# Performance work log

Measured on AMD Instinct MI355X. Metric: run time of the kernel, lower is better.

## Reference

```python
import jax, jax.numpy as jnp
import numpy as np
from jax import lax

B, C, H, W = 2, 96, 64, 64
D_INNER, D_STATE, DT_RANK, K = 192, 16, 6, 4
EPS = 1e-5


def _ln(x, g, b):
    mu = jnp.mean(x, -1, keepdims=True)
    var = jnp.var(x, -1, keepdims=True)
    return (x - mu) * lax.rsqrt(var + EPS) * g + b


def setup_inputs() -> dict:
    key = jax.random.key(0)
    ks = jax.random.split(key, 10)
    f = lambda k, s, sc=0.02: jax.random.normal(k, s, dtype=jnp.float32) * sc
    return {
        "rgb": jax.random.normal(ks[0], (B, C, H, W), dtype=jnp.float32),
        "t": jax.random.normal(ks[1], (B, C, H, W), dtype=jnp.float32),
        "conv_w": f(ks[2], (C, 2 * C, 3, 3), 0.05),
        "conv_b": jnp.zeros((C,), jnp.float32),
        "bn_gamma": jnp.ones((C,), jnp.float32),
        "bn_beta": jnp.zeros((C,), jnp.float32),
        "bn_mean": jnp.zeros((C,), jnp.float32),
        "bn_var": jnp.ones((C,), jnp.float32),
        "ln_gamma": jnp.ones((C,), jnp.float32),
        "ln_beta": jnp.zeros((C,), jnp.float32),
        "in_proj_w": f(ks[3], (2 * D_INNER, C)),
        "dwconv_w": f(ks[4], (D_INNER, 1, 3, 3), 0.1),
        "dwconv_b": jnp.zeros((D_INNER,), jnp.float32),
        "x_proj_w": f(ks[5], (K, DT_RANK + 2 * D_STATE, D_INNER)),
        "dt_w": f(ks[6], (K, D_INNER, DT_RANK), 0.1),
        "dt_b": jnp.full((K, D_INNER), float(np.log(np.expm1(0.01))), jnp.float32),
        "A_logs": jnp.log(jnp.tile(jnp.arange(1, D_STATE + 1, dtype=jnp.float32), (K * D_INNER, 1))),
        "Ds": jnp.ones((K * D_INNER,), jnp.float32),
        "out_norm_gamma": jnp.ones((D_INNER,), jnp.float32),
        "out_norm_beta": jnp.zeros((D_INNER,), jnp.float32),
        "out_proj_w": f(ks[7], (C, D_INNER)),
    }


def _forward(rgb, t, conv_w, conv_b, bn_gamma, bn_beta, bn_mean, bn_var,
             ln_gamma, ln_beta, in_proj_w, dwconv_w, dwconv_b, x_proj_w,
             dt_w, dt_b, A_logs, Ds, out_norm_gamma, out_norm_beta, out_proj_w):
    dn = ("NCHW", "OIHW", "NCHW")
    # BasicConv: conv + BN(eval) + ReLU (dropout inactive in eval)
    x = jnp.concatenate([rgb, t], axis=1)
    x = lax.conv_general_dilated(x, conv_w, (1, 1), "SAME", dimension_numbers=dn)
    x = x + conv_b[None, :, None, None]
    x = (x - bn_mean[None, :, None, None]) * lax.rsqrt(bn_var[None, :, None, None] + EPS)
    x = x * bn_gamma[None, :, None, None] + bn_beta[None, :, None, None]
    x = jax.nn.relu(x)
    # permute to (B,H,W,C) and LayerNorm over channels
    x = _ln(jnp.transpose(x, (0, 2, 3, 1)), ln_gamma, ln_beta)
    # ---- SS2D ----
    xz = jnp.einsum("bhwc,ec->bhwe", x, in_proj_w)  # e = 2*d_inner
    xc, z = jnp.split(xz, 2, axis=-1)
    xc = jnp.transpose(xc, (0, 3, 1, 2))  # (B, d_inner, H, W)
    xc = lax.conv_general_dilated(xc, dwconv_w, (1, 1), "SAME",
                                  dimension_numbers=dn, feature_group_count=D_INNER)
    xc = jax.nn.silu(xc + dwconv_b[None, :, None, None])
    L = H * W
    # cross-scan: row-major, col-major, and their reverses -> (B,4,d,L)
    x_flat = xc.reshape(B, D_INNER, L)
    x_tr = jnp.transpose(xc, (0, 1, 3, 2)).reshape(B, D_INNER, L)
    xs = jnp.stack([x_flat, x_tr], axis=1)
    xs = jnp.concatenate([xs, xs[..., ::-1]], axis=1)  # (B,K,d,L)
    x_dbl = jnp.einsum("bkdl,kcd->bkcl", xs, x_proj_w)
    dts = x_dbl[:, :, :DT_RANK]
    Bs = x_dbl[:, :, DT_RANK:DT_RANK + D_STATE]  # (B,K,N,L)
    Cs = x_dbl[:, :, DT_RANK + D_STATE:]         # (B,K,N,L)
    dts = jnp.einsum("bkrl,kdr->bkdl", dts, dt_w)
    A = -jnp.exp(A_logs).reshape(K, D_INNER, D_STATE)
    Dsk = Ds.reshape(K, D_INNER)
    delta = jax.nn.softplus(dts + dt_b[None, :, :, None])  # (B,K,d,L)
    du = delta * xs

    def step(h, inp):
        dl, dul, Bl, Cl = inp  # (B,K,d),(B,K,d),(B,K,N),(B,K,N)
        h = h * jnp.exp(dl[..., None] * A) + dul[..., None] * Bl[:, :, None, :]
        y = jnp.einsum("bkdn,bkn->bkd", h, Cl)
        return h, y

    h0 = jnp.zeros((B, K, D_INNER, D_STATE), delta.dtype)
    _, ys = lax.scan(step, h0, (
        jnp.transpose(delta, (3, 0, 1, 2)),
        jnp.transpose(du, (3, 0, 1, 2)),
        jnp.transpose(Bs, (3, 0, 1, 2)),
        jnp.transpose(Cs, (3, 0, 1, 2)),
    ))
    out_y = jnp.transpose(ys, (1, 2, 3, 0)) + xs * Dsk[None, :, :, None]  # (B,K,d,L)
    # merge four scan directions back to row-major order
    inv_y = out_y[:, 2:4, :, ::-1]
    wh_y = jnp.transpose(out_y[:, 1].reshape(B, D_INNER, W, H), (0, 1, 3, 2)).reshape(B, D_INNER, L)
    invwh_y = jnp.transpose(inv_y[:, 1].reshape(B, D_INNER, W, H), (0, 1, 3, 2)).reshape(B, D_INNER, L)
    y = out_y[:, 0] + inv_y[:, 0] + wh_y + invwh_y  # (B,d,L)
    y = jnp.transpose(y, (0, 2, 1)).reshape(B, H, W, D_INNER)
    y = _ln(y, out_norm_gamma, out_norm_beta)
    y = y * jax.nn.silu(z)
    out = jnp.einsum("bhwd,cd->bhwc", y, out_proj_w)
    return jnp.transpose(out, (0, 3, 1, 2))  # (B,C,H,W)


def reference(rgb, t, conv_w, conv_b, bn_gamma, bn_beta, bn_mean, bn_var,
              ln_gamma, ln_beta, in_proj_w, dwconv_w, dwconv_b, x_proj_w,
              dt_w, dt_b, A_logs, Ds, out_norm_gamma, out_norm_beta, out_proj_w):
    return _forward(rgb, t, conv_w, conv_b, bn_gamma, bn_beta, bn_mean, bn_var,
                    ln_gamma, ln_beta, in_proj_w, dwconv_w, dwconv_b, x_proj_w,
                    dt_w, dt_b, A_logs, Ds, out_norm_gamma, out_norm_beta, out_proj_w)
```

## Files before the change

### kernel.cpp

```cpp
#include <hip/hip_runtime.h>
#include <math.h>

#define HW 4096
#define CC 96
#define DD 192
#define NS 16
#define KK 4
#define LC 64
#define NC 64
#define NCH (8*DD*NS)

__device__ __forceinline__ float siluf(float x){ return x / (1.f + expf(-x)); }
__device__ __forceinline__ float softplus_fast(float x){ return (x > 20.f) ? x : log1pf(__expf(x)); }

__device__ __forceinline__ int lmap_xs(int k, int l){
  if (k == 1) return ((l & 63) << 6) | (l >> 6);
  if (k == 2) return (HW - 1) - l;
  if (k == 3) { int r = (HW - 1) - l; return ((r & 63) << 6) | (r >> 6); }
  return l;
}

__global__ void k_wprep(const float* __restrict__ cw, float* __restrict__ wT){
  int o = blockIdx.x*256 + threadIdx.x;
  int co = o % 96; int rest = o / 96; int tap = rest % 9; int cig = rest / 9;
  wT[o] = cw[((size_t)co*192 + cig)*9 + tap];
}

__global__ void k_xwprep(const float* __restrict__ xpw, float* __restrict__ xpwT){
  int o = blockIdx.x*256 + threadIdx.x;
  if (o >= 4*192*38) return;
  int c = o % 38; int rest = o / 38; int d = rest % 192; int k = rest / 192;
  xpwT[o] = xpw[((size_t)(k*38 + c))*192 + d];
}

__global__ void __launch_bounds__(256, 4)
k_conv1(const float* __restrict__ rgb, const float* __restrict__ tt,
        const float* __restrict__ wT, float* __restrict__ pbuf){
  __shared__ float in_lds[6][6][68];
  __shared__ __align__(16) float w_lds[6][9][64];
  int bi = blockIdx.x;
  int kc  = bi & 15;        int ci0 = kc*12;
  int cog = (bi >> 4) & 1;  int co0 = cog*48;
  int b   = (bi >> 5) & 1;
  int pt  = bi >> 6;        int h0 = pt*4;
  int tid = threadIdx.x;
  int pg = tid & 31;  int r = pg >> 3;  int w0 = (pg & 7)*8;
  int cg = tid >> 5;  int co_t = cg*6;

  float acc[6][8];
  #pragma unroll
  for (int c = 0; c < 6; ++c)
    #pragma unroll
    for (int p = 0; p < 8; ++p) acc[c][p] = 0.f;

  for (int s = 0; s < 2; ++s){
    if (s) __syncthreads();
    if (tid < 72){ int side = tid & 1; int rr = (tid % 12) >> 1; int ci = tid / 12;
                   in_lds[ci][rr][side ? 65 : 0] = 0.f; }
    for (int i = tid; i < 2304; i += 256){
      int ci = i / 384; int rem = i - ci*384; int rr = rem >> 6; int w = rem & 63;
      int grow = h0 - 1 + rr;
      int cig = ci0 + s*6 + ci;
      float v = 0.f;
      if (grow >= 0 && grow < 64){
        const float* src = (cig < CC) ? (rgb + (size_t)(b*CC+cig)*HW)
                                      : (tt  + (size_t)(b*CC+cig-CC)*HW);
        v = src[grow*64 + w];
      }
      in_lds[ci][rr][w+1] = v;
    }
    for (int i = tid; i < 2592; i += 256){
      int co = i % 48; int rest = i / 48; int tap = rest % 9; int ci = rest / 9;
      w_lds[ci][tap][(co/6)*8 + (co%6)] =
          wT[((size_t)(ci0 + s*6 + ci)*9 + tap)*96 + co0 + co];
    }
    __syncthreads();
    #pragma unroll
    for (int ci = 0; ci < 6; ++ci){
      float rowv[3][10];
      #pragma unroll
      for (int rr = 0; rr < 3; ++rr){
        const float* rp = &in_lds[ci][r+rr][w0];
        float4 a = *(const float4*)rp;
        float4 bb = *(const float4*)(rp+4);
        float2 cc = *(const float2*)(rp+8);
        rowv[rr][0]=a.x; rowv[rr][1]=a.y; rowv[rr][2]=a.z; rowv[rr][3]=a.w;
        rowv[rr][4]=bb.x; rowv[rr][5]=bb.y; rowv[rr][6]=bb.z; rowv[rr][7]=bb.w;
        rowv[rr][8]=cc.x; rowv[rr][9]=cc.y;
      }
      #pragma unroll
      for (int tap = 0; tap < 9; ++tap){
        int rt = tap/3, ct = tap - rt*3;
        float4 wa = *(const float4*)&w_lds[ci][tap][cg*8];
        float2 wb = *(const float2*)&w_lds[ci][tap][cg*8+4];
        float wv[6] = {wa.x, wa.y, wa.z, wa.w, wb.x, wb.y};
        #pragma unroll
        for (int p = 0; p < 8; ++p){
          float iv = rowv[rt][p + ct];
          #pragma unroll
          for (int c = 0; c < 6; ++c) acc[c][p] += wv[c]*iv;
        }
      }
    }
  }
  #pragma unroll
  for (int p = 0; p < 8; ++p){
    int pix = (h0 + r)*64 + w0 + p;
    float* o = pbuf + (((size_t)kc*2 + b)*HW + pix)*CC + co0 + co_t;
    float2 o0 = {acc[0][p], acc[1][p]};
    float2 o1 = {acc[2][p], acc[3][p]};
    float2 o2 = {acc[4][p], acc[5][p]};
    *(float2*)&o[0] = o0; *(float2*)&o[2] = o1; *(float2*)&o[4] = o2;
  }
}

__global__ void k_convred(const float* __restrict__ pbuf, const float* __restrict__ cb,
                          const float* __restrict__ bng, const float* __restrict__ bnb,
                          const float* __restrict__ bnm, const float* __restrict__ bnv,
                          const float* __restrict__ lng, const float* __restrict__ lnb,
                          float* __restrict__ xn){
  __shared__ float sm[4], sm2[4], smu[2], srs[2];
  int tid = threadIdx.x;
  int half = tid >> 7;
  int c = tid & 127;
  int pixg = blockIdx.x*2 + half;
  int b = pixg >> 12; int pix = pixg & (HW-1);
  float v = 0.f;
  if (c < CC){
    #pragma unroll
    for (int kc = 0; kc < 16; ++kc)
      v += pbuf[(((size_t)kc*2 + b)*HW + pix)*CC + c];
    v += cb[c];
    v = (v - bnm[c]) * rsqrtf(bnv[c] + 1e-5f);
    v = v * bng[c] + bnb[c];
    v = fmaxf(v, 0.f);
  }
  float s = v, s2 = v*v;
  #pragma unroll
  for (int off = 32; off; off >>= 1){ s += __shfl_down(s, off); s2 += __shfl_down(s2, off); }
  if ((tid & 63) == 0){ sm[tid>>6] = s; sm2[tid>>6] = s2; }
  __syncthreads();
  if (tid < 2){
    float ts = sm[2*tid] + sm[2*tid+1];
    float ts2 = sm2[2*tid] + sm2[2*tid+1];
    float mu = ts * (1.f/CC);
    float var = ts2 * (1.f/CC) - mu*mu;
    smu[tid] = mu; srs[tid] = rsqrtf(var + 1e-5f);
  }
  __syncthreads();
  if (c < CC)
    xn[(size_t)pixg*CC + c] = (v - smu[half])*srs[half]*lng[c] + lnb[c];
}

__global__ void k_inproj(const float* __restrict__ xn, const float* __restrict__ ipw,
                         float* __restrict__ xz){
  __shared__ float As[64][97];
  __shared__ __align__(16) float Bs[96][68];
  int p0 = blockIdx.x*64;
  int e0 = blockIdx.y*64;
  int tid = threadIdx.x;
  for (int idx = tid; idx < 64*96; idx += 256){
    int r = idx/96, c = idx - r*96;
    As[r][c] = xn[(size_t)(p0+r)*96 + c];
  }
  for (int idx = tid; idx < 96*64; idx += 256){
    int c = idx/64, e = idx - c*64;
    Bs[c][e] = ipw[(size_t)(e0+e)*96 + c];
  }
  __syncthreads();
  int tx = tid & 15, ty = tid >> 4;
  float acc[4][4] = {};
  for (int c = 0; c < 96; ++c){
    float a[4];
    #pragma unroll
    for (int i = 0; i < 4; ++i) a[i] = As[ty*4+i][c];
    float4 bb = *(const float4*)&Bs[c][tx*4];
    float bv[4] = {bb.x, bb.y, bb.z, bb.w};
    #pragma unroll
    for (int i = 0; i < 4; ++i)
      #pragma unroll
      for (int j = 0; j < 4; ++j) acc[i][j] += a[i]*bv[j];
  }
  for (int i = 0; i < 4; ++i){
    float4 o = {acc[i][0], acc[i][1], acc[i][2], acc[i][3]};
    *(float4*)&xz[(size_t)(p0+ty*4+i)*384 + e0 + tx*4] = o;
  }
}

__global__ void k_dwconv(const float* __restrict__ xz, const float* __restrict__ dww,
                         const float* __restrict__ dwb, float* __restrict__ xc){
  int gid = blockIdx.x*256 + threadIdx.x;
  int dq = gid % 48; int bp = gid / 48;
  int d = dq*4;
  int pix = bp & (HW-1); int b = bp >> 12;
  int h = pix >> 6, w = pix & 63;
  float4 acc = *(const float4*)&dwb[d];
  float wreg[4][9];
  #pragma unroll
  for (int j = 0; j < 4; ++j)
    #pragma unroll
    for (int t = 0; t < 9; ++t) wreg[j][t] = dww[(d+j)*9 + t];
  #pragma unroll
  for (int dh = -1; dh <= 1; ++dh){
    int hh = h + dh;
    if (hh < 0 || hh > 63) continue;
    #pragma unroll
    for (int dw2 = -1; dw2 <= 1; ++dw2){
      int ww = w + dw2;
      if (ww < 0 || ww > 63) continue;
      float4 v = *(const float4*)&xz[((size_t)b*HW + hh*64 + ww)*384 + d];
      int t = (dh+1)*3 + (dw2+1);
      acc.x += v.x*wreg[0][t];
      acc.y += v.y*wreg[1][t];
      acc.z += v.z*wreg[2][t];
      acc.w += v.w*wreg[3][t];
    }
  }
  float4 o = {siluf(acc.x), siluf(acc.y), siluf(acc.z), siluf(acc.w)};
  *(float4*)&xc[(size_t)bp*DD + d] = o;
}

__global__ void __launch_bounds__(320)
k_xdbl(const float* __restrict__ xc, const float* __restrict__ xpwT,
       float* __restrict__ Bsb, float* __restrict__ Csb, float* __restrict__ dtsG){
  __shared__ float xs_t[48*36];
  __shared__ float w_t[48*80];
  int blk = blockIdx.x;
  int lt = blk & 127; int p = (blk >> 7) & 1; int b = blk >> 8;
  int l0 = lt*32;
  int tid = threadIdx.x;
  int lg = tid & 15, cg = tid >> 4;
  int c0 = cg*4;
  int b4kA = b*4 + p, b4kB = b*4 + p + 2;

  float acc[4][2] = {};
  for (int ch = 0; ch < 4; ++ch){
    int d0 = ch*48;
    if (ch) __syncthreads();
    for (int i = tid; i < 384; i += 320){
      int j = i & 31; int dq = i >> 5;
      int l = l0 + j;
      int lm = (p == 0) ? l : (((l & 63) << 6) | (l >> 6));
      float4 v = *(const float4*)&xc[((size_t)b*HW + lm)*DD + d0 + dq*4];
      xs_t[(dq*4+0)*36 + j] = v.x;
      xs_t[(dq*4+1)*36 + j] = v.y;
      xs_t[(dq*4+2)*36 + j] = v.z;
      xs_t[(dq*4+3)*36 + j] = v.w;
    }
    for (int i = tid; i < 3648; i += 320){
      int c = i % 76; int dd = i / 76;
      int kk = (c < 38) ? p : (p + 2);
      int cc = (c < 38) ? c : c - 38;
      w_t[dd*80 + c] = xpwT[((size_t)kk*192 + d0 + dd)*38 + cc];
    }
    __syncthreads();
    #pragma unroll 4
    for (int dd = 0; dd < 48; ++dd){
      float4 wv = *(const float4*)&w_t[dd*80 + c0];
      float2 xv = *(const float2*)&xs_t[dd*36 + lg*2];
      acc[0][0] += wv.x*xv.x; acc[0][1] += wv.x*xv.y;
      acc[1][0] += wv.y*xv.x; acc[1][1] += wv.y*xv.y;
      acc[2][0] += wv.z*xv.x; acc[2][1] += wv.z*xv.y;
      acc[3][0] += wv.w*xv.x; acc[3][1] += wv.w*xv.y;
    }
  }
  #pragma unroll
  for (int j = 0; j < 4; ++j){
    int c = c0 + j;
    #pragma unroll
    for (int i = 0; i < 2; ++i){
      float v = acc[j][i];
      int lf = l0 + lg*2 + i;
      int lr = HW - 1 - lf;
      if      (c <  6) dtsG[((size_t)b4kA*HW + lf)*8 + c]        = v;
      else if (c < 22) Bsb [((size_t)b4kA*HW + lf)*NS + (c-6)]   = v;
      else if (c < 38) Csb [((size_t)b4kA*HW + lf)*NS + (c-22)]  = v;
      else if (c < 44) dtsG[((size_t)b4kB*HW + lr)*8 + (c-38)]   = v;
      else if (c < 60) Bsb [((size_t)b4kB*HW + lr)*NS + (c-44)]  = v;
      else if (c < 76) Csb [((size_t)b4kB*HW + lr)*NS + (c-60)]  = v;
    }
  }
}

__global__ void __launch_bounds__(192)
k_dt(const float* __restrict__ dtsG, const float* __restrict__ dtw,
     const float* __restrict__ dtb, float* __restrict__ dlt){
  int blk = blockIdx.x;
  int lt = blk & 511; int b4k = blk >> 9;
  int k = b4k & 3;
  int d = threadIdx.x;
  int l0 = lt*8;
  const float* wp = &dtw[(size_t)(k*DD + d)*6];
  float w0=wp[0], w1=wp[1], w2=wp[2], w3=wp[3], w4=wp[4], w5=wp[5];
  float bias = dtb[k*DD + d];
  #pragma unroll
  for (int j = 0; j < 8; ++j){
    const float* tp = &dtsG[((size_t)b4k*HW + l0 + j)*8];
    float4 t0 = *(const float4*)tp;
    float2 t1 = *(const float2*)(tp+4);
    float s = bias + t0.x*w0 + t0.y*w1 + t0.z*w2 + t0.w*w3 + t1.x*w4 + t1.y*w5;
    dlt[((size_t)b4k*HW + l0 + j)*DD + d] = softplus_fast(s);
  }
}

__global__ void k_scan1(const float* __restrict__ dlt, const float* __restrict__ xc,
                        const float* __restrict__ Bsb, const float* __restrict__ Alog,
                        float* __restrict__ Ac, float* __restrict__ Bc){
  int tid = blockIdx.x*256 + threadIdx.x;
  int ng = tid & 3;
  int t2 = tid >> 2;
  int d = t2 % DD;
  int rest = t2 / DD;
  int chunk = rest & (NC-1);
  int b4k = rest >> 6;
  int k = b4k & 3, b = b4k >> 2;
  float4 Af = *(const float4*)&Alog[(size_t)(k*DD+d)*NS + ng*4];
  float Av[4] = {-expf(Af.x), -expf(Af.y), -expf(Af.z), -expf(Af.w)};
  float h[4] = {0.f,0.f,0.f,0.f};
  float ap[4] = {1.f,1.f,1.f,1.f};
  int l0 = chunk*LC;
  const float* dp  = dlt + ((size_t)b4k*HW + l0)*DD + d;
  const float4* Bp4 = (const float4*)(Bsb + ((size_t)b4k*HW + l0)*NS) + ng;
  const float* xcb = xc + (size_t)b*HW*DD + d;
  float dvc = dp[0];
  float xvc = xcb[(size_t)lmap_xs(k, l0)*DD];
  float4 Bvc = Bp4[0];
  #pragma unroll 4
  for (int i = 0; i < LC; ++i){
    float dvn = 0.f, xvn = 0.f; float4 Bvn = {0.f,0.f,0.f,0.f};
    if (i+1 < LC){
      dvn = dp[(size_t)(i+1)*DD];
      xvn = xcb[(size_t)lmap_xs(k, l0+i+1)*DD];
      Bvn = Bp4[(size_t)(i+1)*4];
    }
    float du = dvc*xvc;
    float a0 = __expf(dvc*Av[0]), a1 = __expf(dvc*Av[1]),
          a2 = __expf(dvc*Av[2]), a3 = __expf(dvc*Av[3]);
    h[0] = h[0]*a0 + du*Bvc.x; ap[0] *= a0;
    h[1] = h[1]*a1 + du*Bvc.y; ap[1] *= a1;
    h[2] = h[2]*a2 + du*Bvc.z; ap[2] *= a2;
    h[3] = h[3]*a3 + du*Bvc.w; ap[3] *= a3;
    dvc = dvn; xvc = xvn; Bvc = Bvn;
  }
  size_t base = (size_t)chunk*NCH + (size_t)(b4k*DD + d)*NS + ng*4;
  *(float4*)&Ac[base] = make_float4(ap[0],ap[1],ap[2],ap[3]);
  *(float4*)&Bc[base] = make_float4(h[0],h[1],h[2],h[3]);
}

__global__ void k_scan2(float* __restrict__ Ac, const float* __restrict__ Bc){
  int chain = blockIdx.x*256 + threadIdx.x;
  float h = 0.f;
  for (int c = 0; c < NC; ++c){
    size_t idx = (size_t)c*NCH + chain;
    float a = Ac[idx], bv = Bc[idx];
    Ac[idx] = h;
    h = a*h + bv;
  }
}

__global__ void k_scan3(const float* __restrict__ dlt, const float* __restrict__ xc,
                        const float* __restrict__ Bsb, const float* __restrict__ Csb,
                        const float* __restrict__ Alog, const float* __restrict__ hst,
                        float* __restrict__ ys){
  int tid = blockIdx.x*256 + threadIdx.x;
  int ng = tid & 3;
  int t2 = tid >> 2;
  int d = t2 % DD;
  int rest = t2 / DD;
  int chunk = rest & (NC-1);
  int b4k = rest >> 6;
  int k = b4k & 3, b = b4k >> 2;
  float4 Af = *(const float4*)&Alog[(size_t)(k*DD+d)*NS + ng*4];
  float Av[4] = {-expf(Af.x), -expf(Af.y), -expf(Af.z), -expf(Af.w)};
  size_t hbase = (size_t)chunk*NCH + (size_t)(b4k*DD + d)*NS + ng*4;
  float4 hf = *(const float4*)&hst[hbase];
  float h[4] = {hf.x, hf.y, hf.z, hf.w};
  int l0 = chunk*LC;
  const float* dp  = dlt + ((size_t)b4k*HW + l0)*DD + d;
  const float4* Bp4 = (const float4*)(Bsb + ((size_t)b4k*HW + l0)*NS) + ng;
  const float4* Cp4 = (const float4*)(Csb + ((size_t)b4k*HW + l0)*NS) + ng;
  const float* xcb = xc + (size_t)b*HW*DD + d;
  float* yp = ys + ((size_t)b4k*HW + l0)*DD + d;
  float dvc = dp[0];
  float xvc = xcb[(size_t)lmap_xs(k, l0)*DD];
  float4 Bvc = Bp4[0];
  float4 Cvc = Cp4[0];
  #pragma unroll 4
  for (int i = 0; i < LC; ++i){
    float dvn = 0.f, xvn = 0.f; float4 Bvn = {0.f,0.f,0.f,0.f}, Cvn = {0.f,0.f,0.f,0.f};
    if (i+1 < LC){
      dvn = dp[(size_t)(i+1)*DD];
      xvn = xcb[(size_t)lmap_xs(k, l0+i+1)*DD];
      Bvn = Bp4[(size_t)(i+1)*4];
      Cvn = Cp4[(size_t)(i+1)*4];
    }
    float du = dvc*xvc;
    float a0 = __expf(dvc*Av[0]), a1 = __expf(dvc*Av[1]),
          a2 = __expf(dvc*Av[2]), a3 = __expf(dvc*Av[3]);
    h[0] = h[0]*a0 + du*Bvc.x;
    h[1] = h[1]*a1 + du*Bvc.y;
    h[2] = h[2]*a2 + du*Bvc.z;
    h[3] = h[3]*a3 + du*Bvc.w;
    float y = h[0]*Cvc.x + h[1]*Cvc.y + h[2]*Cvc.z + h[3]*Cvc.w;
    y += __shfl_xor(y, 1, 4);
    y += __shfl_xor(y, 2, 4);
    if (ng == 0) yp[(size_t)i*DD] = y;
    dvc = dvn; xvc = xvn; Bvc = Bvn; Cvc = Cvn;
  }
}

__global__ void k_gate(const float* __restrict__ ys, const float* __restrict__ xc,
                       const float* __restrict__ Ds, const float* __restrict__ xz,
                       const float* __restrict__ ong, const float* __restrict__ onb,
                       float* __restrict__ yg){
  int gt = blockIdx.x*256 + threadIdx.x;
  int wave = gt >> 6;
  int lane = gt & 63;
  int b = wave >> 12; int l = wave & (HW-1);
  int l1 = ((l & 63) << 6) | (l >> 6);
  size_t base = (size_t)b*KK*HW*DD;
  float v[3]; float s = 0.f, s2 = 0.f;
  #pragma unroll
  for (int j = 0; j < 3; ++j){
    int d = lane + j*64;
    float t;
    t  = ys[base + ((size_t)0*HW + l        )*DD + d];
    t += ys[base + ((size_t)1*HW + l1       )*DD + d];
    t += ys[base + ((size_t)2*HW + (HW-1-l ))*DD + d];
    t += ys[base + ((size_t)3*HW + (HW-1-l1))*DD + d];
    t += xc[((size_t)b*HW + l)*DD + d] * (Ds[d] + Ds[DD+d] + Ds[2*DD+d] + Ds[3*DD+d]);
    v[j] = t; s += t; s2 += t*t;
  }
  #pragma unroll
  for (int off = 32; off; off >>= 1){ s += __shfl_xor(s, off); s2 += __shfl_xor(s2, off); }
  float mu = s*(1.f/DD);
  float rstd = rsqrtf(s2*(1.f/DD) - mu*mu + 1e-5f);
  #pragma unroll
  for (int j = 0; j < 3; ++j){
    int d = lane + j*64;
    float z = xz[((size_t)b*HW + l)*384 + DD + d];
    float x = (v[j]-mu)*rstd*ong[d] + onb[d];
    yg[(size_t)wave*DD + d] = x * siluf(z);
  }
}

__global__ void k_outproj(const float* __restrict__ yg, const float* __restrict__ opw,
                          float* __restrict__ out){
  __shared__ float yl[48][36];
  __shared__ float wl[48][97];
  int blk = blockIdx.x;
  int b = blk >> 7; int pt = blk & 127;
  int px0 = pt*32;
  int tid = threadIdx.x;
  int pxg = tid & 7;
  int cgi = tid >> 3;
  float acc[4][3] = {};
  for (int k0 = 0; k0 < DD; k0 += 48){
    if (k0) __syncthreads();
    for (int i = tid; i < 32*48; i += 256){
      int r = i/48, k = i - r*48;
      yl[k][r] = yg[((size_t)b*HW + px0 + r)*DD + k0 + k];
    }
    for (int i = tid; i < 96*48; i += 256){
      int c = i/48, k = i - c*48;
      wl[k][c] = opw[(size_t)c*DD + k0 + k];
    }
    __syncthreads();
    #pragma unroll 4
    for (int k = 0; k < 48; ++k){
      float4 yv = *(const float4*)&yl[k][pxg*4];
      float w0 = wl[k][cgi*3], w1 = wl[k][cgi*3+1], w2 = wl[k][cgi*3+2];
      acc[0][0] += yv.x*w0; acc[0][1] += yv.x*w1; acc[0][2] += yv.x*w2;
      acc[1][0] += yv.y*w0; acc[1][1] += yv.y*w1; acc[1][2] += yv.y*w2;
      acc[2][0] += yv.z*w0; acc[2][1] += yv.z*w1; acc[2][2] += yv.z*w2;
      acc[3][0] += yv.w*w0; acc[3][1] += yv.w*w1; acc[3][2] += yv.w*w2;
    }
  }
  #pragma unroll
  for (int j = 0; j < 3; ++j){
    int c = cgi*3 + j;
    float4 o = {acc[0][j], acc[1][j], acc[2][j], acc[3][j]};
    *(float4*)&out[((size_t)b*CC + c)*HW + px0 + pxg*4] = o;
  }
}

extern "C" void kernel_launch(void* const* d_in, const int* in_sizes, int n_in,
                              void* d_out, int out_size, void* d_ws, size_t ws_size,
                              hipStream_t stream) {
  const float* rgb   = (const float*)d_in[0];
  const float* tt    = (const float*)d_in[1];
  const float* cw    = (const float*)d_in[2];
  const float* cb    = (const float*)d_in[3];
  const float* bng   = (const float*)d_in[4];
  const float* bnb   = (const float*)d_in[5];
  const float* bnm   = (const float*)d_in[6];
  const float* bnv   = (const float*)d_in[7];
  const float* lng   = (const float*)d_in[8];
  const float* lnb   = (const float*)d_in[9];
  const float* ipw   = (const float*)d_in[10];
  const float* dww   = (const float*)d_in[11];
  const float* dwb   = (const float*)d_in[12];
  const float* xpw   = (const float*)d_in[13];
  const float* dtw   = (const float*)d_in[14];
  const float* dtb   = (const float*)d_in[15];
  const float* Alog  = (const float*)d_in[16];
  const float* Ds    = (const float*)d_in[17];
  const float* ong   = (const float*)d_in[18];
  const float* onb   = (const float*)d_in[19];
  const float* opw   = (const float*)d_in[20];
  float* out = (float*)d_out;

  float* ws = (float*)d_ws;
  float* xn   = ws + 786432;
  float* xz   = ws + 1572864;
  float* xc   = ws + 4718592;
  float* Bsb  = ws + 6291456;
  float* Csb  = ws + 6815744;
  float* dlt  = ws + 7340032;
  float* ysb  = ws + 13631488;
  float* dtsG = ws;
  float* pbuf = ws + 1572864;
  float* Ac   = ws;
  float* Bc   = ysb;
  float* yg   = ws + 7340032;
  float* wT   = ws + 16777216;
  float* xpwT = ws + 16943104;

  k_wprep<<<648, 256, 0, stream>>>(cw, wT);
  k_xwprep<<<114, 256, 0, stream>>>(xpw, xpwT);
  k_conv1<<<1024, 256, 0, stream>>>(rgb, tt, wT, pbuf);
  k_convred<<<4096, 256, 0, stream>>>(pbuf, cb, bng, bnb, bnm, bnv, lng, lnb, xn);
  dim3 g2(128, 6);
  k_inproj<<<g2, 256, 0, stream>>>(xn, ipw, xz);
  k_dwconv<<<1536, 256, 0, stream>>>(xz, dww, dwb, xc);
  k_xdbl<<<512, 320, 0, stream>>>(xc, xpwT, Bsb, Csb, dtsG);
  k_dt<<<4096, 192, 0, stream>>>(dtsG, dtw, dtb, dlt);
  k_scan1<<<1536, 256, 0, stream>>>(dlt, xc, Bsb, Alog, Ac, Bc);
  k_scan2<<<96, 256, 0, stream>>>(Ac, Bc);
  k_scan3<<<1536, 256, 0, stream>>>(dlt, xc, Bsb, Csb, Alog, Ac, ysb);
  k_gate<<<2048, 256, 0, stream>>>(ysb, xc, Ds, xz, ong, onb, yg);
  k_outproj<<<256, 256, 0, stream>>>(yg, opw, out);
}
```

Baseline: 254.6 us.

## Retile conv1 with register-prefetch double staging and fewer channel splits

Each conv1 block now covers 2 output rows instead of 4 and 24 input channels in four stages instead of 12 in two. The split-K factor drops from 16 to 8, which halves the partial-sum buffer that the reduction kernel writes and reads. Inputs and weights for the next stage are prefetched into registers while the current stage computes, then written to LDS between barriers. In exchange each thread holds fewer accumulators, there is more halo overhead per row, and extra barriers are added.

```diff
diff --git a/kernel.cpp b/kernel.cpp
--- a/kernel.cpp
+++ b/kernel.cpp
@@ -33,60 +33,88 @@
   xpwT[o] = xpw[((size_t)(k*38 + c))*192 + d];
 }
 
-__global__ void __launch_bounds__(256, 4)
+__global__ void __launch_bounds__(256, 2)
 k_conv1(const float* __restrict__ rgb, const float* __restrict__ tt,
         const float* __restrict__ wT, float* __restrict__ pbuf){
-  __shared__ float in_lds[6][6][68];
+  __shared__ __align__(16) float in_lds[6][4][68];
   __shared__ __align__(16) float w_lds[6][9][64];
   int bi = blockIdx.x;
-  int kc  = bi & 15;        int ci0 = kc*12;
-  int cog = (bi >> 4) & 1;  int co0 = cog*48;
-  int b   = (bi >> 5) & 1;
-  int pt  = bi >> 6;        int h0 = pt*4;
+  int kc  = bi & 7;         int ci0 = kc*24;
+  int cog = (bi >> 3) & 1;  int co0 = cog*48;
+  int b   = (bi >> 4) & 1;
+  int pt  = bi >> 5;        int h0 = pt*2;
   int tid = threadIdx.x;
-  int pg = tid & 31;  int r = pg >> 3;  int w0 = (pg & 7)*8;
+  int pg = tid & 31;  int r = pg >> 4;  int w0 = (pg & 15)*4;
   int cg = tid >> 5;  int co_t = cg*6;
 
-  float acc[6][8];
-  #pragma unroll
-  for (int c = 0; c < 6; ++c)
-    #pragma unroll
-    for (int p = 0; p < 8; ++p) acc[c][p] = 0.f;
-
-  for (int s = 0; s < 2; ++s){
-    if (s) __syncthreads();
-    if (tid < 72){ int side = tid & 1; int rr = (tid % 12) >> 1; int ci = tid / 12;
-                   in_lds[ci][rr][side ? 65 : 0] = 0.f; }
-    for (int i = tid; i < 2304; i += 256){
-      int ci = i / 384; int rem = i - ci*384; int rr = rem >> 6; int w = rem & 63;
-      int grow = h0 - 1 + rr;
-      int cig = ci0 + s*6 + ci;
+  if (tid < 48){ int side = tid & 1; int rr = (tid >> 1) & 3; int ci = tid >> 3;
+                 in_lds[ci][rr][side ? 65 : 0] = 0.f; }
+
+  float inreg[6], wreg[11];
+  auto load_in = [&](int s){
+    #pragma unroll
+    for (int j = 0; j < 6; ++j){
+      int i = tid + j*256;
+      int ci = i >> 8; int rem = i & 255;
+      int rr = rem >> 6; int w = rem & 63;
+      int grow = h0 - 1 + rr; int cig = ci0 + s*6 + ci;
       float v = 0.f;
       if (grow >= 0 && grow < 64){
         const float* src = (cig < CC) ? (rgb + (size_t)(b*CC+cig)*HW)
                                       : (tt  + (size_t)(b*CC+cig-CC)*HW);
         v = src[grow*64 + w];
       }
-      in_lds[ci][rr][w+1] = v;
-    }
-    for (int i = tid; i < 2592; i += 256){
-      int co = i % 48; int rest = i / 48; int tap = rest % 9; int ci = rest / 9;
-      w_lds[ci][tap][(co/6)*8 + (co%6)] =
-          wT[((size_t)(ci0 + s*6 + ci)*9 + tap)*96 + co0 + co];
-    }
-    __syncthreads();
+      inreg[j] = v;
+    }
+    #pragma unroll
+    for (int j = 0; j < 11; ++j){
+      int i = tid + j*256;
+      if (i < 2592){
+        int co = i % 48; int rest = i / 48; int tap = rest % 9; int ci = rest / 9;
+        wreg[j] = wT[((size_t)(ci0 + s*6 + ci)*9 + tap)*96 + co0 + co];
+      }
+    }
+  };
+  auto write_stage = [&](){
+    #pragma unroll
+    for (int j = 0; j < 6; ++j){
+      int i = tid + j*256;
+      int ci = i >> 8; int rem = i & 255;
+      int rr = rem >> 6; int w = rem & 63;
+      in_lds[ci][rr][w+1] = inreg[j];
+    }
+    #pragma unroll
+    for (int j = 0; j < 11; ++j){
+      int i = tid + j*256;
+      if (i < 2592){
+        int co = i % 48; int rest = i / 48; int tap = rest % 9; int ci = rest / 9;
+        w_lds[ci][tap][(co/6)*8 + (co%6)] = wreg[j];
+      }
+    }
+  };
+
+  float acc[6][4];
+  #pragma unroll
+  for (int c = 0; c < 6; ++c)
+    #pragma unroll
+    for (int p = 0; p < 4; ++p) acc[c][p] = 0.f;
+
+  load_in(0);
+  write_stage();
+  __syncthreads();
+
+  for (int s = 0; s < 4; ++s){
+    if (s < 3) load_in(s+1);
     #pragma unroll
     for (int ci = 0; ci < 6; ++ci){
-      float rowv[3][10];
+      float rowv[3][6];
       #pragma unroll
       for (int rr = 0; rr < 3; ++rr){
         const float* rp = &in_lds[ci][r+rr][w0];
         float4 a = *(const float4*)rp;
-        float4 bb = *(const float4*)(rp+4);
-        float2 cc = *(const float2*)(rp+8);
+        float2 c2 = *(const float2*)(rp+4);
         rowv[rr][0]=a.x; rowv[rr][1]=a.y; rowv[rr][2]=a.z; rowv[rr][3]=a.w;
-        rowv[rr][4]=bb.x; rowv[rr][5]=bb.y; rowv[rr][6]=bb.z; rowv[rr][7]=bb.w;
-        rowv[rr][8]=cc.x; rowv[rr][9]=cc.y;
+        rowv[rr][4]=c2.x; rowv[rr][5]=c2.y;
       }
       #pragma unroll
       for (int tap = 0; tap < 9; ++tap){
@@ -95,16 +123,22 @@
         float2 wb = *(const float2*)&w_lds[ci][tap][cg*8+4];
         float wv[6] = {wa.x, wa.y, wa.z, wa.w, wb.x, wb.y};
         #pragma unroll
-        for (int p = 0; p < 8; ++p){
+        for (int p = 0; p < 4; ++p){
           float iv = rowv[rt][p + ct];
           #pragma unroll
           for (int c = 0; c < 6; ++c) acc[c][p] += wv[c]*iv;
         }
       }
     }
-  }
-  #pragma unroll
-  for (int p = 0; p < 8; ++p){
+    if (s < 3){
+      __syncthreads();
+      write_stage();
+      __syncthreads();
+    }
+  }
+
+  #pragma unroll
+  for (int p = 0; p < 4; ++p){
     int pix = (h0 + r)*64 + w0 + p;
     float* o = pbuf + (((size_t)kc*2 + b)*HW + pix)*CC + co0 + co_t;
     float2 o0 = {acc[0][p], acc[1][p]};
@@ -128,7 +162,7 @@
   float v = 0.f;
   if (c < CC){
     #pragma unroll
-    for (int kc = 0; kc < 16; ++kc)
+    for (int kc = 0; kc < 8; ++kc)
       v += pbuf[(((size_t)kc*2 + b)*HW + pix)*CC + c];
     v += cb[c];
     v = (v - bnm[c]) * rsqrtf(bnv[c] + 1e-5f);
```

New measurement: 616.6 us. 2.42x slower.
